# Performance work log

Hardware: AMD Instinct MI355X
Metric: run time of the kernel (lower is better)

## Reference

```python
import jax, jax.numpy as jnp
import numpy as np

TEMPERATURE = 6.0
NOISE_STD_MIN = 0.3
NOISE_STD_MAX = 0.9
CLIP_MAX = 0.6
ROUND_FACTOR = 10.0  # 10 ** round_digit, round_digit = 1
EPS = 1e-4

BATCH = 32768
NUM_CLASSES = 1000


def setup_inputs() -> dict:
    key = jax.random.key(0)
    k1, k2, k3 = jax.random.split(key, 3)
    logits = jax.random.normal(k1, (BATCH, NUM_CLASSES), dtype=jnp.float32) * 3.0
    noise = jax.random.normal(k2, (BATCH, NUM_CLASSES), dtype=jnp.float32)
    u = jax.random.uniform(k3, (BATCH, 1), dtype=jnp.float32)
    return {"logits": logits, "noise": noise, "u": u}


def reference(logits, noise, u):
    # Layer 2: temperature scaling
    raw = logits / TEMPERATURE                                   # [B, C]
    # Layer 3: adaptive noise, std depends on max confidence
    probs_tmp = jax.nn.softmax(raw, axis=1)
    max_conf = jnp.max(probs_tmp, axis=1, keepdims=True)          # [B, 1]
    std = NOISE_STD_MIN + (NOISE_STD_MAX - NOISE_STD_MIN) * max_conf ** 2
    noisy = raw + noise * std
    # Layer 4: clip, renormalize, round
    probs = jax.nn.softmax(noisy, axis=1)
    probs = jnp.clip(probs, 0.0, CLIP_MAX)
    probs = probs / jnp.sum(probs, axis=1, keepdims=True)
    probs = jnp.round(probs * ROUND_FACTOR) / ROUND_FACTOR
    C = probs.shape[1]
    # rows that rounded to all-zero become uniform
    row_sum = jnp.sum(probs, axis=1, keepdims=True)               # [B, 1]
    probs = jnp.where(row_sum == 0, 1.0 / C, probs)
    # multinomial(num_samples=1) via inverse-CDF with provided uniform u
    cum = jnp.cumsum(probs, axis=1)                               # [B, C]
    thresh = u * cum[:, -1:]                                      # unnormalized CDF sampling
    idx = jnp.sum(cum < thresh, axis=1)                           # [B] int32
    one_hot = jax.nn.one_hot(idx, C, dtype=probs.dtype)
    sanitised_logits = jnp.log(one_hot * (1.0 - EPS) + EPS / C)
    return sanitised_logits
```

## Files before the change

### kernel.cpp

```cpp
#include <hip/hip_runtime.h>
#include <math.h>

#define NCLS 1000
#define NF4  250
#define TPB  256
#define WPB  4

typedef float vfloat4 __attribute__((ext_vector_type(4)));

#if __has_builtin(__builtin_amdgcn_exp2f)
__device__ __forceinline__ float fast_exp2(float x) { return __builtin_amdgcn_exp2f(x); }
#else
__device__ __forceinline__ float fast_exp2(float x) { return exp2f(x); }
#endif

__device__ __forceinline__ float scan_val(int k) {
    const unsigned xb = __float_as_uint(0.001f);
    const int hb = 31 - __clz(k);
    float acc = __uint_as_float(xb + ((unsigned)hb << 23));
    #pragma unroll 1
    for (int l = hb - 1; l >= 0; --l) {
        if (k & (1u << l)) {
            const float t = __uint_as_float(xb + ((unsigned)l << 23));
            acc += t;
            asm volatile("" : "+v"(acc));
        }
    }
    return acc;
}

__device__ __forceinline__ int count_below(float th) {
    int k0 = (int)fmaf(th, 1000.0f, 0.5f);
    k0 = (k0 < 1) ? 1 : (k0 > 1000 ? 1000 : k0);
    return (k0 - 1) + ((scan_val(k0) < th) ? 1 : 0);
}

__device__ __forceinline__ float wave_max(float v) {
    #pragma unroll
    for (int o = 32; o; o >>= 1) v = fmaxf(v, __shfl_xor(v, o));
    return v;
}
__device__ __forceinline__ float wave_sum(float v) {
    #pragma unroll
    for (int o = 32; o; o >>= 1) v += __shfl_xor(v, o);
    return v;
}
__device__ __forceinline__ int wave_sumi(int v) {
    #pragma unroll
    for (int o = 32; o; o >>= 1) v += __shfl_xor(v, o);
    return v;
}

__global__ __launch_bounds__(TPB, 8) void defence_kernel(
    const float* __restrict__ logits,
    const float* __restrict__ noise,
    const float* __restrict__ u,
    float* __restrict__ out,
    int batch)
{
    const int lane = threadIdx.x & 63;
    const int wid  = threadIdx.x >> 6;
    const int row  = blockIdx.x * WPB + wid;
    if (row >= batch) return;

    __shared__ unsigned char kbuf[WPB][NCLS];

    const float uu = u[row];

    const float NEG = -INFINITY;
    const vfloat4* lg4 = reinterpret_cast<const vfloat4*>(logits + (size_t)row * NCLS);
    const vfloat4* nz4 = reinterpret_cast<const vfloat4*>(noise  + (size_t)row * NCLS);

    vfloat4 lv[4], nv[4];
    #pragma unroll
    for (int t = 0; t < 4; ++t) {
        const int j = lane + 64 * t;
        const bool a = j < NF4;
        if (a) {
            lv[t] = __builtin_nontemporal_load(&lg4[j]);
            nv[t] = __builtin_nontemporal_load(&nz4[j]);
        } else {
            lv[t] = (vfloat4){NEG, NEG, NEG, NEG};
            nv[t] = (vfloat4){0.f, 0.f, 0.f, 0.f};
        }
    }

    const float T999 = scan_val(1000);
    const float th0  = uu * T999;
    int idx = count_below(th0);

    const float V0 = logf(1e-7f);
    const float V1 = logf(0.9999f + 1e-7f);
    vfloat4* o4 = reinterpret_cast<vfloat4*>(out + (size_t)row * NCLS);
    #pragma unroll
    for (int t = 0; t < 4; ++t) {
        const int j = lane + 64 * t;
        if (j < NF4) {
            vfloat4 ov = {V0, V0, V0, V0};
            const int base = 4 * j;
            if (idx >= base && idx < base + 4)
                ov[idx - base] = V1;
            __builtin_nontemporal_store(ov, &o4[j]);
        }
    }

    const float K6 = 0.2404491734814939f;
    float mA = NEG, sA = 0.f;
    #pragma unroll
    for (int t = 0; t < 4; ++t) {
        mA = fmaxf(mA, fmaxf(fmaxf(lv[t][0], lv[t][1]), fmaxf(lv[t][2], lv[t][3])));
        sA += (fast_exp2(lv[t][0] * K6) + fast_exp2(lv[t][1] * K6))
            + (fast_exp2(lv[t][2] * K6) + fast_exp2(lv[t][3] * K6));
    }
    const float m1 = wave_max(mA);
    const float s1 = wave_sum(sA);
    const float mc = fast_exp2(m1 * K6) / s1;
    const float sd = fmaf(0.6f, mc * mc, 0.3f);

    const float L2E = 1.4426950408889634f;
    float m2l = NEG, s2l = 0.f;
    #pragma unroll
    for (int t = 0; t < 4; ++t) {
        const float y0 = fmaf(nv[t][0], sd, lv[t][0] * (1.0f / 6.0f));
        const float y1 = fmaf(nv[t][1], sd, lv[t][1] * (1.0f / 6.0f));
        const float y2 = fmaf(nv[t][2], sd, lv[t][2] * (1.0f / 6.0f));
        const float y3 = fmaf(nv[t][3], sd, lv[t][3] * (1.0f / 6.0f));
        m2l = fmaxf(m2l, fmaxf(fmaxf(y0, y1), fmaxf(y2, y3)));
        s2l += (fast_exp2(y0 * L2E) + fast_exp2(y1 * L2E))
             + (fast_exp2(y2 * L2E) + fast_exp2(y3 * L2E));
    }
    const float m2  = wave_max(m2l);
    const float s2  = wave_sum(s2l);
    const float e2m = fast_exp2(m2 * L2E);

    if (__builtin_expect(!(s2 > 22.0f * e2m), 0)) {
        const float m1x = m1 / 6.0f;
        float se1 = 0.f;
        #pragma unroll
        for (int t = 0; t < 4; ++t)
            se1 += expf(lv[t][0] / 6.0f - m1x) + expf(lv[t][1] / 6.0f - m1x)
                 + expf(lv[t][2] / 6.0f - m1x) + expf(lv[t][3] / 6.0f - m1x);
        const float s1x = wave_sum(se1);
        const float mcx = 1.0f / s1x;
        const float sdx = 0.3f + 0.6f * (mcx * mcx);

        float m2xl = NEG;
        #pragma unroll
        for (int t = 0; t < 4; ++t) {
            const float y0 = lv[t][0] / 6.0f + nv[t][0] * sdx;
            const float y1 = lv[t][1] / 6.0f + nv[t][1] * sdx;
            const float y2 = lv[t][2] / 6.0f + nv[t][2] * sdx;
            const float y3 = lv[t][3] / 6.0f + nv[t][3] * sdx;
            m2xl = fmaxf(m2xl, fmaxf(fmaxf(y0, y1), fmaxf(y2, y3)));
        }
        const float m2x = wave_max(m2xl);
        float se2 = 0.f;
        #pragma unroll
        for (int t = 0; t < 4; ++t)
            se2 += expf(lv[t][0] / 6.0f + nv[t][0] * sdx - m2x)
                 + expf(lv[t][1] / 6.0f + nv[t][1] * sdx - m2x)
                 + expf(lv[t][2] / 6.0f + nv[t][2] * sdx - m2x)
                 + expf(lv[t][3] / 6.0f + nv[t][3] * sdx - m2x);
        const float s2x = wave_sum(se2);
        float cs = 0.f;
        #pragma unroll
        for (int t = 0; t < 4; ++t)
            cs += fminf(expf(lv[t][0] / 6.0f + nv[t][0] * sdx - m2x) / s2x, 0.6f)
                + fminf(expf(lv[t][1] / 6.0f + nv[t][1] * sdx - m2x) / s2x, 0.6f)
                + fminf(expf(lv[t][2] / 6.0f + nv[t][2] * sdx - m2x) / s2x, 0.6f)
                + fminf(expf(lv[t][3] / 6.0f + nv[t][3] * sdx - m2x) / s2x, 0.6f);
        const float rsum = wave_sum(cs);
        int kls = 0;
        #pragma unroll
        for (int t = 0; t < 4; ++t) {
            const int j = lane + 64 * t;
            if (j < NF4) {
                const float yv[4] = {
                    lv[t][0] / 6.0f + nv[t][0] * sdx, lv[t][1] / 6.0f + nv[t][1] * sdx,
                    lv[t][2] / 6.0f + nv[t][2] * sdx, lv[t][3] / 6.0f + nv[t][3] * sdx };
                #pragma unroll
                for (int c = 0; c < 4; ++c) {
                    const float cl = fminf(expf(yv[c] - m2x) / s2x, 0.6f);
                    const int kk = (int)rintf((cl / rsum) * 10.0f);
                    kbuf[wid][4 * j + c] = (unsigned char)kk;
                    kls += kk;
                }
            }
        }
        const int K = wave_sumi(kls);
        int idx2;
        if (K == 0) {
            idx2 = count_below(th0);
        } else {
            asm volatile("s_waitcnt lgkmcnt(0)" ::: "memory");
            __builtin_amdgcn_wave_barrier();
            int cnt = 0;
            if (lane == 0) {
                const double tab[11] = {0.0, 0.1, 0.2, 0.3, 0.4, 0.5,
                                        0.6, 0.7, 0.8, 0.9, 1.0};
                double c = 0.0;
                for (int i = 0; i < NCLS; ++i) c += tab[kbuf[wid][i]];
                const double th = (double)uu * c;
                c = 0.0;
                for (int i = 0; i < NCLS; ++i) {
                    c += tab[kbuf[wid][i]];
                    cnt += (c < th) ? 1 : 0;
                }
            }
            idx2 = __shfl(cnt, 0);
        }
        #pragma unroll
        for (int t = 0; t < 4; ++t) {
            const int j = lane + 64 * t;
            if (j < NF4) {
                vfloat4 ov = {V0, V0, V0, V0};
                const int base = 4 * j;
                if (idx2 >= base && idx2 < base + 4)
                    ov[idx2 - base] = V1;
                __builtin_nontemporal_store(ov, &o4[j]);
            }
        }
    }
}

extern "C" void kernel_launch(void* const* d_in, const int* in_sizes, int n_in,
                              void* d_out, int out_size, void* d_ws, size_t ws_size,
                              hipStream_t stream) {
    const float* logits = (const float*)d_in[0];
    const float* noise  = (const float*)d_in[1];
    const float* u      = (const float*)d_in[2];
    float* out = (float*)d_out;

    const int batch = in_sizes[2];
    const int blocks = (batch + WPB - 1) / WPB;

    hipLaunchKernelGGL(defence_kernel, dim3(blocks), dim3(TPB), 0, stream,
                       logits, noise, u, out, batch);
}
```

Baseline: 70.47 us.

## Split output writing into a separate kernel ahead of the input-verification kernel

The speculative uniform-row output write moves into its own writer kernel, which only reads u and stores the one-hot log row. A second kernel reads logits and noise and rewrites a row only when the fallback check fires. Output stores change from nontemporal to regular stores. The aim is to separate write traffic from read traffic, possibly leaving the output resident in cache. The cost is an extra launch and no overlap of reads and writes within one kernel.

```diff
diff --git a/kernel.cpp b/kernel.cpp
--- a/kernel.cpp
+++ b/kernel.cpp
@@ -51,7 +51,37 @@
     return v;
 }
 
-__global__ __launch_bounds__(TPB, 8) void defence_kernel(
+__global__ __launch_bounds__(TPB, 8) void writer_kernel(
+    const float* __restrict__ u,
+    float* __restrict__ out,
+    int batch)
+{
+    const int lane = threadIdx.x & 63;
+    const int wid  = threadIdx.x >> 6;
+    const int row  = blockIdx.x * WPB + wid;
+    if (row >= batch) return;
+
+    const float T999 = scan_val(1000);
+    const float th0  = u[row] * T999;
+    const int idx = count_below(th0);
+
+    const float V0 = logf(1e-7f);
+    const float V1 = logf(0.9999f + 1e-7f);
+    vfloat4* o4 = reinterpret_cast<vfloat4*>(out + (size_t)row * NCLS);
+    #pragma unroll
+    for (int t = 0; t < 4; ++t) {
+        const int j = lane + 64 * t;
+        if (j < NF4) {
+            vfloat4 ov = {V0, V0, V0, V0};
+            const int base = 4 * j;
+            if (idx >= base && idx < base + 4)
+                ov[idx - base] = V1;
+            o4[j] = ov;
+        }
+    }
+}
+
+__global__ __launch_bounds__(TPB, 8) void verify_kernel(
     const float* __restrict__ logits,
     const float* __restrict__ noise,
     const float* __restrict__ u,
@@ -65,8 +95,6 @@
 
     __shared__ unsigned char kbuf[WPB][NCLS];
 
-    const float uu = u[row];
-
     const float NEG = -INFINITY;
     const vfloat4* lg4 = reinterpret_cast<const vfloat4*>(logits + (size_t)row * NCLS);
     const vfloat4* nz4 = reinterpret_cast<const vfloat4*>(noise  + (size_t)row * NCLS);
@@ -75,32 +103,12 @@
     #pragma unroll
     for (int t = 0; t < 4; ++t) {
         const int j = lane + 64 * t;
-        const bool a = j < NF4;
-        if (a) {
+        if (j < NF4) {
             lv[t] = __builtin_nontemporal_load(&lg4[j]);
             nv[t] = __builtin_nontemporal_load(&nz4[j]);
         } else {
             lv[t] = (vfloat4){NEG, NEG, NEG, NEG};
             nv[t] = (vfloat4){0.f, 0.f, 0.f, 0.f};
-        }
-    }
-
-    const float T999 = scan_val(1000);
-    const float th0  = uu * T999;
-    int idx = count_below(th0);
-
-    const float V0 = logf(1e-7f);
-    const float V1 = logf(0.9999f + 1e-7f);
-    vfloat4* o4 = reinterpret_cast<vfloat4*>(out + (size_t)row * NCLS);
-    #pragma unroll
-    for (int t = 0; t < 4; ++t) {
-        const int j = lane + 64 * t;
-        if (j < NF4) {
-            vfloat4 ov = {V0, V0, V0, V0};
-            const int base = 4 * j;
-            if (idx >= base && idx < base + 4)
-                ov[idx - base] = V1;
-            __builtin_nontemporal_store(ov, &o4[j]);
         }
     }
 
@@ -134,6 +142,7 @@
     const float e2m = fast_exp2(m2 * L2E);
 
     if (__builtin_expect(!(s2 > 22.0f * e2m), 0)) {
+        const float uu = u[row];
         const float m1x = m1 / 6.0f;
         float se1 = 0.f;
         #pragma unroll
@@ -190,7 +199,7 @@
         const int K = wave_sumi(kls);
         int idx2;
         if (K == 0) {
-            idx2 = count_below(th0);
+            idx2 = count_below(uu * scan_val(1000));
         } else {
             asm volatile("s_waitcnt lgkmcnt(0)" ::: "memory");
             __builtin_amdgcn_wave_barrier();
@@ -209,6 +218,9 @@
             }
             idx2 = __shfl(cnt, 0);
         }
+        const float V0 = logf(1e-7f);
+        const float V1 = logf(0.9999f + 1e-7f);
+        vfloat4* o4 = reinterpret_cast<vfloat4*>(out + (size_t)row * NCLS);
         #pragma unroll
         for (int t = 0; t < 4; ++t) {
             const int j = lane + 64 * t;
@@ -217,7 +229,7 @@
                 const int base = 4 * j;
                 if (idx2 >= base && idx2 < base + 4)
                     ov[idx2 - base] = V1;
-                __builtin_nontemporal_store(ov, &o4[j]);
+                o4[j] = ov;
             }
         }
     }
@@ -234,6 +246,8 @@
     const int batch = in_sizes[2];
     const int blocks = (batch + WPB - 1) / WPB;
 
-    hipLaunchKernelGGL(defence_kernel, dim3(blocks), dim3(TPB), 0, stream,
+    hipLaunchKernelGGL(writer_kernel, dim3(blocks), dim3(TPB), 0, stream,
+                       u, out, batch);
+    hipLaunchKernelGGL(verify_kernel, dim3(blocks), dim3(TPB), 0, stream,
                        logits, noise, u, out, batch);
 }
```

Measured after the change: 66.17 us. 6.1% less time.
